# Kernel tuning notes

Hardware: AMD Instinct MI355X
Metric: run time of the kernel (lower is better)

## Reference

```python
import math
import jax, jax.numpy as jnp
import numpy as np

B, N, D, E = 4, 256, 256, 128  # batch, nodes, node_dim, edge_dim


def setup_inputs() -> dict:
    key = jax.random.key(0)
    ks = jax.random.split(key, 12)
    s_d = 1.0 / math.sqrt(D)
    s_e = 1.0 / math.sqrt(E)
    s_3d = 1.0 / math.sqrt(3 * D)
    return {
        "h": jax.random.normal(ks[0], (B, N, D), jnp.float32),
        "g": jax.random.normal(ks[1], (B, N, N, E), jnp.float32),
        "node_mask": jnp.ones((B, N), dtype=bool),
        # attention projections (stored as (in, out); x @ W == torch Linear)
        "Wq": jax.random.normal(ks[2], (D, D), jnp.float32) * s_d,
        "Wk": jax.random.normal(ks[3], (E, D), jnp.float32) * s_e,
        "Wv": jax.random.normal(ks[4], (E, D), jnp.float32) * s_e,
        # edge_to_node MLP: Linear(D,D) -> SiLU -> Linear(D,D)
        "W1a": jax.random.normal(ks[5], (D, D), jnp.float32) * s_d,
        "b1a": jnp.zeros((D,), jnp.float32),
        "W2a": jax.random.normal(ks[6], (D, D), jnp.float32) * s_d,
        "b2a": jnp.zeros((D,), jnp.float32),
        # node_to_edge MLP: Linear(3D,E) -> SiLU -> Linear(E,E)
        "W1b": jax.random.normal(ks[7], (3 * D, E), jnp.float32) * s_3d,
        "b1b": jnp.zeros((E,), jnp.float32),
        "W2b": jax.random.normal(ks[8], (E, E), jnp.float32) * s_e,
        "b2b": jnp.zeros((E,), jnp.float32),
    }


def reference(h, g, node_mask, Wq, Wk, Wv, W1a, b1a, W2a, b2a, W1b, b1b, W2b, b2b):
    scale = 1.0 / math.sqrt(D)
    # Edge-to-Node attention
    q = h @ Wq                                   # (B,N,D)
    k = jnp.einsum('bije,ed->bijd', g, Wk)       # (B,N,N,D)
    v = jnp.einsum('bije,ed->bijd', g, Wv)       # (B,N,N,D)
    scores = jnp.einsum('bid,bijd->bij', q, k) * scale
    edge_mask = node_mask[:, :, None] & node_mask[:, None, :]
    scores = jnp.where(edge_mask, scores, -10000.0)
    alpha = jax.nn.softmax(scores, axis=2)
    alpha = alpha * node_mask[:, :, None].astype(alpha.dtype)
    node_agg = jnp.einsum('bij,bijd->bid', alpha, v)
    # edge_to_node MLP (dropout = identity at inference)
    h_update = h + (jax.nn.silu(node_agg @ W1a + b1a) @ W2a + b2a)
    # Node-to-Edge: split W1b so the (B,N,N,3D) concat is never materialized;
    # pair @ W1b == h_i @ Wi + h_j @ Wj + (h_i*h_j) @ Wh  (mathematically identical)
    Wi, Wj, Wh = W1b[:D], W1b[D:2 * D], W1b[2 * D:]
    xi = (h_update @ Wi)[:, :, None, :]          # (B,N,1,E)
    xj = (h_update @ Wj)[:, None, :, :]          # (B,1,N,E)
    had = h_update[:, :, None, :] * h_update[:, None, :, :]  # (B,N,N,D)
    pre = xi + xj + jnp.einsum('bijd,de->bije', had, Wh) + b1b
    g_update = g + (jax.nn.silu(pre) @ W2b + b2b)
    return (h_update, g_update)
```

## Files before the change

### kernel.cpp

```cpp
#include <hip/hip_runtime.h>

typedef unsigned short u16;
typedef short short8 __attribute__((ext_vector_type(8)));
typedef float f32x4 __attribute__((ext_vector_type(4)));

#define DEV __device__ __forceinline__

DEV float bf2f(u16 u) { return __uint_as_float(((unsigned int)u) << 16); }
DEV u16 f2bf(float f) {
    unsigned int u = __float_as_uint(f);
    u += 0x7fffu + ((u >> 16) & 1u);
    return (u16)(u >> 16);
}
DEV unsigned cvtpk_bf16(float lo, float hi) {
    unsigned r;
    asm("v_cvt_pk_bf16_f32 %0, %1, %2" : "=v"(r) : "v"(lo), "v"(hi));
    return r;
}
DEV float sigf(float x) { return 1.0f / (1.0f + __expf(-x)); }

__global__ __launch_bounds__(256) void k_prep_t(const float* __restrict__ W1b,
                                                const float* __restrict__ W2b,
                                                u16* __restrict__ WhT,
                                                u16* __restrict__ W2bT) {
    __shared__ u16 sT[64 * 72];
    int t = threadIdx.x, blk = blockIdx.x;
    const float* src;
    u16* dst;
    int R, C, ri, ci;
    if (blk < 8) {
        src = W1b + 512 * 128;
        dst = WhT;
        R = 256; C = 128;
        ri = blk >> 1; ci = blk & 1;
    } else {
        src = W2b; dst = W2bT; R = 128; C = 128;
        int lb = blk - 8;
        ri = lb >> 1; ci = lb & 1;
    }
    int lr = t >> 2, q = t & 3;
#pragma unroll
    for (int s4 = 0; s4 < 4; ++s4) {
        float4 v = *(const float4*)(src + (size_t)(ri * 64 + lr) * C + ci * 64 + q * 16 + s4 * 4);
        int c0 = q * 16 + s4 * 4;
        sT[(c0 + 0) * 72 + lr] = f2bf(v.x);
        sT[(c0 + 1) * 72 + lr] = f2bf(v.y);
        sT[(c0 + 2) * 72 + lr] = f2bf(v.z);
        sT[(c0 + 3) * 72 + lr] = f2bf(v.w);
    }
    __syncthreads();
    int dr = t >> 2;
#pragma unroll
    for (int s8 = 0; s8 < 2; ++s8) {
        int cc = q * 16 + s8 * 8;
        ushort4 w0, w1;
        w0.x = sT[dr * 72 + cc + 0]; w0.y = sT[dr * 72 + cc + 1];
        w0.z = sT[dr * 72 + cc + 2]; w0.w = sT[dr * 72 + cc + 3];
        w1.x = sT[dr * 72 + cc + 4]; w1.y = sT[dr * 72 + cc + 5];
        w1.z = sT[dr * 72 + cc + 6]; w1.w = sT[dr * 72 + cc + 7];
        *(ushort4*)(dst + (size_t)(ci * 64 + dr) * R + ri * 64 + cc) = w0;
        *(ushort4*)(dst + (size_t)(ci * 64 + dr) * R + ri * 64 + cc + 4) = w1;
    }
}

__global__ __launch_bounds__(128) void k_prep_m1(const float* __restrict__ Wq,
                                                 const float* __restrict__ Wk,
                                                 float* __restrict__ M1) {
    __shared__ float swq[256];
    int t = threadIdx.x, c = blockIdx.x;
    swq[t] = Wq[c * 256 + t];
    swq[t + 128] = Wq[c * 256 + t + 128];
    __syncthreads();
    const float* wk = Wk + (size_t)t * 256;
    float acc = 0.f;
#pragma unroll 4
    for (int d = 0; d < 256; d += 4) {
        float4 b = *(const float4*)(wk + d);
        acc += swq[d] * b.x + swq[d + 1] * b.y + swq[d + 2] * b.z + swq[d + 3] * b.w;
    }
    M1[c * 128 + t] = acc;
}

__global__ __launch_bounds__(256) void k_prep_m2(const float* __restrict__ Wv,
                                                 const float* __restrict__ W1a,
                                                 float* __restrict__ M2) {
    __shared__ float sv[256];
    int t = threadIdx.x, e = blockIdx.x;
    sv[t] = Wv[(size_t)e * 256 + t];
    __syncthreads();
    float acc = 0.f;
#pragma unroll 16
    for (int d = 0; d < 256; ++d) acc += sv[d] * W1a[d * 256 + t];
    M2[e * 256 + t] = acc;
}

__global__ __launch_bounds__(256) void k_qk(const float* __restrict__ h,
                                            const float* __restrict__ M1,
                                            float* __restrict__ qk) {
    __shared__ float sh[2][256];
    __shared__ float sp[2][2][128];
    int t = threadIdx.x;
    int r0 = blockIdx.x * 2;
    sh[0][t] = h[(size_t)r0 * 256 + t];
    sh[1][t] = h[(size_t)(r0 + 1) * 256 + t];
    __syncthreads();
    int e = t & 127, ch = t >> 7;
    float a0 = 0.f, a1 = 0.f;
    const float* m1 = M1 + (size_t)ch * 128 * 128;
    const float* s0 = &sh[0][ch * 128];
    const float* s1 = &sh[1][ch * 128];
#pragma unroll 16
    for (int c = 0; c < 128; ++c) {
        float m = m1[c * 128 + e];
        a0 += s0[c] * m;
        a1 += s1[c] * m;
    }
    sp[ch][0][e] = a0;
    sp[ch][1][e] = a1;
    __syncthreads();
    if (t < 128) qk[(size_t)r0 * 128 + t] = sp[0][0][t] + sp[1][0][t];
    else qk[(size_t)(r0 + 1) * 128 + (t - 128)] = sp[0][1][t - 128] + sp[1][1][t - 128];
}

__global__ __launch_bounds__(256) void k_attn(const float* __restrict__ g,
                                              const float* __restrict__ qk,
                                              float* __restrict__ gagg) {
    __shared__ __align__(16) u16 sg[32768];
    __shared__ float sqk[128];
    __shared__ float ssc[256];
    __shared__ float sred[4];
    __shared__ float sacc[512];
    int t = threadIdx.x, bi = blockIdx.x;
    int lane = t & 63, wv = t >> 6;
    if (t < 128) sqk[t] = qk[bi * 128 + t] * 0.0625f;
    const float* gb = g + (size_t)bi * 32768;
#pragma unroll
    for (int it = 0; it < 32; ++it) {
        int idx = (it * 256 + t) * 4;
        float4 v = *(const float4*)(gb + idx);
        ushort4 pk;
        pk.x = f2bf(v.x); pk.y = f2bf(v.y); pk.z = f2bf(v.z); pk.w = f2bf(v.w);
        *(ushort4*)(sg + idx) = pk;
    }
    __syncthreads();

    float s = 0.f;
#pragma unroll 8
    for (int it = 0; it < 64; ++it) {
        int p2 = (it + t) & 63;
        unsigned int u = *(const unsigned int*)(sg + t * 128 + 2 * p2);
        float2 qv = *(const float2*)(sqk + 2 * p2);
        s += bf2f((u16)(u & 0xffffu)) * qv.x + bf2f((u16)(u >> 16)) * qv.y;
    }

    float v = s;
#pragma unroll
    for (int off = 32; off > 0; off >>= 1) v = fmaxf(v, __shfl_xor(v, off));
    if (lane == 0) sred[wv] = v;
    __syncthreads();
    float m = fmaxf(fmaxf(sred[0], sred[1]), fmaxf(sred[2], sred[3]));
    float pv = __expf(s - m);
    ssc[t] = pv;
    float sv = pv;
#pragma unroll
    for (int off = 32; off > 0; off >>= 1) sv += __shfl_xor(sv, off);
    __syncthreads();
    if (lane == 0) sred[wv] = sv;
    __syncthreads();
    float s_sum = sred[0] + sred[1] + sred[2] + sred[3];

    int epair = t & 63, jq = t >> 6;
    float a0 = 0.f, a1 = 0.f;
    const u16* sq = sg + jq * 8192 + 2 * epair;
#pragma unroll 8
    for (int jj = 0; jj < 64; ++jj) {
        unsigned int u = *(const unsigned int*)(sq + jj * 128);
        float p = ssc[jq * 64 + jj];
        a0 += p * bf2f((u16)(u & 0xffffu));
        a1 += p * bf2f((u16)(u >> 16));
    }
    sacc[jq * 128 + 2 * epair] = a0;
    sacc[jq * 128 + 2 * epair + 1] = a1;
    __syncthreads();
    if (t < 128)
        gagg[bi * 128 + t] = (sacc[t] + sacc[128 + t] + sacc[256 + t] + sacc[384 + t]) / s_sum;
}

__global__ __launch_bounds__(256) void k_hmlp(
    const float* __restrict__ h, const float* __restrict__ gagg,
    const float* __restrict__ M2, const float* __restrict__ b1a,
    const float* __restrict__ W2a, const float* __restrict__ b2a,
    const float* __restrict__ W1b, const float* __restrict__ b1b,
    float* __restrict__ hu_ws, u16* __restrict__ hub_ws,
    float* __restrict__ xi_ws, float* __restrict__ xj_ws,
    float* __restrict__ out) {
    __shared__ float sgg[2][128];
    __shared__ float su[2][256];
    __shared__ float shu[2][256];
    int t = threadIdx.x;
    int r0 = blockIdx.x * 2;
    sgg[t >> 7][t & 127] = gagg[(size_t)(r0 + (t >> 7)) * 128 + (t & 127)];
    __syncthreads();
    float a0 = b1a[t], a1 = a0;
#pragma unroll 16
    for (int e = 0; e < 128; ++e) {
        float mm = M2[e * 256 + t];
        a0 += sgg[0][e] * mm;
        a1 += sgg[1][e] * mm;
    }
    su[0][t] = a0 * sigf(a0);
    su[1][t] = a1 * sigf(a1);
    __syncthreads();
    float b2av = b2a[t];
    float h0 = h[(size_t)r0 * 256 + t] + b2av;
    float h1 = h[(size_t)(r0 + 1) * 256 + t] + b2av;
#pragma unroll 16
    for (int c = 0; c < 256; ++c) {
        float mm = W2a[c * 256 + t];
        h0 += su[0][c] * mm;
        h1 += su[1][c] * mm;
    }
    shu[0][t] = h0;
    shu[1][t] = h1;
    hu_ws[(size_t)r0 * 256 + t] = h0;
    hu_ws[(size_t)(r0 + 1) * 256 + t] = h1;
    hub_ws[(size_t)r0 * 256 + t] = f2bf(h0);
    hub_ws[(size_t)(r0 + 1) * 256 + t] = f2bf(h1);
    out[(size_t)r0 * 256 + t] = h0;
    out[(size_t)(r0 + 1) * 256 + t] = h1;
    __syncthreads();
    int e = t & 127, which = t >> 7;
    const float* Wp = W1b + (size_t)which * 32768;
    float x0 = which ? 0.f : b1b[e];
    float x1 = x0;
#pragma unroll 16
    for (int c = 0; c < 256; ++c) {
        float mm = Wp[c * 128 + e];
        x0 += shu[0][c] * mm;
        x1 += shu[1][c] * mm;
    }
    float* dst = which ? xj_ws : xi_ws;
    dst[(size_t)r0 * 128 + e] = x0;
    dst[(size_t)(r0 + 1) * 128 + e] = x1;
}

__global__ __launch_bounds__(256, 4) void k_gupd(
    const float* __restrict__ g, const float* __restrict__ hu_ws,
    const u16* __restrict__ hub_ws,
    const float* __restrict__ xi_ws, const float* __restrict__ xj_ws,
    const u16* __restrict__ WhT, const u16* __restrict__ W2bT,
    const float* __restrict__ b2b, float* __restrict__ out) {
    __shared__ __align__(16) u16 sP[128 * 136];
    __shared__ float s_hui[256];
    __shared__ float s_xi[128];

    int t = threadIdx.x;
    int bi = blockIdx.x;
    int jb = blockIdx.y;
    int b = bi >> 8;
    int j0 = jb * 128;
    int w = t >> 6, lane = t & 63, n = lane & 15, quad = lane >> 4;

    s_hui[t] = hu_ws[(size_t)bi * 256 + t];
    if (t < 128) s_xi[t] = xi_ws[(size_t)bi * 128 + t];
    __syncthreads();

    int jr = w * 32 + quad * 4;

    const float* xjp = xj_ws + (size_t)(b * 256 + j0) * 128;
    f32x4 acc[2][8];
#pragma unroll
    for (int mti = 0; mti < 2; ++mti)
#pragma unroll
        for (int et = 0; et < 8; ++et) {
            int e = et * 16 + n;
            float xiv = s_xi[e];
#pragma unroll
            for (int r = 0; r < 4; ++r)
                acc[mti][et][r] = xiv + xjp[(size_t)(jr + mti * 16 + r) * 128 + e];
        }

    const u16* hub = hub_ws + (size_t)(b * 256 + j0) * 256;
    int row0 = w * 32 + n;
#pragma unroll
    for (int kc = 0; kc < 4; ++kc) {
#pragma unroll
        for (int s = 0; s < 2; ++s) {
            int c0 = kc * 64 + s * 32 + quad * 8;
            short8 hj0 = *(const short8*)(hub + (size_t)row0 * 256 + c0);
            short8 hj1 = *(const short8*)(hub + (size_t)(row0 + 16) * 256 + c0);
            float4 hA = *(const float4*)(s_hui + c0);
            float4 hB = *(const float4*)(s_hui + c0 + 4);
            float hi8[8] = {hA.x, hA.y, hA.z, hA.w, hB.x, hB.y, hB.z, hB.w};
            union { short8 s8; unsigned u[4]; } a0v, a1v;
#pragma unroll
            for (int k = 0; k < 4; ++k) {
                a0v.u[k] = cvtpk_bf16(bf2f((u16)hj0[2 * k]) * hi8[2 * k],
                                      bf2f((u16)hj0[2 * k + 1]) * hi8[2 * k + 1]);
                a1v.u[k] = cvtpk_bf16(bf2f((u16)hj1[2 * k]) * hi8[2 * k],
                                      bf2f((u16)hj1[2 * k + 1]) * hi8[2 * k + 1]);
            }
#pragma unroll
            for (int et = 0; et < 8; ++et) {
                short8 bfr = *(const short8*)(WhT + (size_t)(et * 16 + n) * 256 + c0);
                acc[0][et] = __builtin_amdgcn_mfma_f32_16x16x32_bf16(a0v.s8, bfr, acc[0][et], 0, 0, 0);
                acc[1][et] = __builtin_amdgcn_mfma_f32_16x16x32_bf16(a1v.s8, bfr, acc[1][et], 0, 0, 0);
            }
        }
    }

#pragma unroll
    for (int mti = 0; mti < 2; ++mti)
#pragma unroll
        for (int et = 0; et < 8; ++et)
#pragma unroll
            for (int r = 0; r < 4; ++r) {
                float x = acc[mti][et][r];
                sP[(w * 32 + mti * 16 + quad * 4 + r) * 136 + et * 16 + n] = f2bf(x * sigf(x));
            }
    __syncthreads();

#pragma unroll
    for (int et = 0; et < 8; ++et) {
        float bv = b2b[et * 16 + n];
        f32x4 iv = {bv, bv, bv, bv};
        acc[0][et] = iv;
        acc[1][et] = iv;
    }
#pragma unroll
    for (int ks = 0; ks < 4; ++ks) {
        int f0 = ks * 32;
        short8 a0 = *(const short8*)(sP + (w * 32 + n) * 136 + f0 + quad * 8);
        short8 a1 = *(const short8*)(sP + (w * 32 + 16 + n) * 136 + f0 + quad * 8);
#pragma unroll
        for (int et = 0; et < 8; ++et) {
            short8 bfr = *(const short8*)(W2bT + (size_t)(et * 16 + n) * 128 + f0 + quad * 8);
            acc[0][et] = __builtin_amdgcn_mfma_f32_16x16x32_bf16(a0, bfr, acc[0][et], 0, 0, 0);
            acc[1][et] = __builtin_amdgcn_mfma_f32_16x16x32_bf16(a1, bfr, acc[1][et], 0, 0, 0);
        }
    }

    const float* gbase = g + ((size_t)bi * 256 + j0) * 128;
    float* obase = out + 262144 + ((size_t)bi * 256 + j0) * 128;
#pragma unroll
    for (int mti = 0; mti < 2; ++mti) {
        float gv[32];
#pragma unroll
        for (int et = 0; et < 8; ++et)
#pragma unroll
            for (int r = 0; r < 4; ++r)
                gv[et * 4 + r] = gbase[(size_t)(jr + mti * 16 + r) * 128 + et * 16 + n];
#pragma unroll
        for (int et = 0; et < 8; ++et)
#pragma unroll
            for (int r = 0; r < 4; ++r)
                obase[(size_t)(jr + mti * 16 + r) * 128 + et * 16 + n] =
                    gv[et * 4 + r] + acc[mti][et][r];
    }
}

extern "C" void kernel_launch(void* const* d_in, const int* in_sizes, int n_in,
                              void* d_out, int out_size, void* d_ws, size_t ws_size,
                              hipStream_t stream) {
    const float* h   = (const float*)d_in[0];
    const float* g   = (const float*)d_in[1];
    const float* Wq  = (const float*)d_in[3];
    const float* Wk  = (const float*)d_in[4];
    const float* Wv  = (const float*)d_in[5];
    const float* W1a = (const float*)d_in[6];
    const float* b1a = (const float*)d_in[7];
    const float* W2a = (const float*)d_in[8];
    const float* b2a = (const float*)d_in[9];
    const float* W1b = (const float*)d_in[10];
    const float* b1b = (const float*)d_in[11];
    const float* W2b = (const float*)d_in[12];
    const float* b2b = (const float*)d_in[13];

    float* ws   = (float*)d_ws;
    float* M1   = ws;
    float* M2   = M1 + 32768;
    float* qk   = M2 + 32768;
    float* xj   = qk;
    float* gagg = qk + 131072;
    float* hu   = gagg + 131072;
    float* xi   = hu + 262144;
    u16* hub    = (u16*)(xi + 131072);
    u16* WhT    = hub + 262144;
    u16* W2bT   = WhT + 32768;

    float* out = (float*)d_out;

    k_prep_t<<<12, 256, 0, stream>>>(W1b, W2b, WhT, W2bT);
    k_prep_m1<<<256, 128, 0, stream>>>(Wq, Wk, M1);
    k_prep_m2<<<128, 256, 0, stream>>>(Wv, W1a, M2);
    k_qk<<<512, 256, 0, stream>>>(h, M1, qk);
    k_attn<<<1024, 256, 0, stream>>>(g, qk, gagg);
    k_hmlp<<<512, 256, 0, stream>>>(h, gagg, M2, b1a, W2a, b2a, W1b, b1b,
                                    hu, hub, xi, xj, out);
    k_gupd<<<dim3(1024, 2), 256, 0, stream>>>(g, hu, hub, xi, xj, WhT, W2bT, b2b, out);
}
```

Baseline: 454.0 us.

## Fold xj projection into gupd MFMA loop and stage g-update epilogue through LDS

The h_j @ Wj term is no longer precomputed in fp32 by the node MLP kernel and reloaded per tile. It is now computed inside the edge-update kernel with extra bf16 MFMAs against a newly transposed WjT, reusing the already-loaded h_j fragments. This removes the scattered fp32 xj loads, at the cost of extra MFMA work per tile and bf16 precision for that term. Separately, the final g + delta write now stages the accumulators through shared memory, so global g reads and output writes become coalesced float4 accesses. That costs extra barriers and shared-memory traffic.

```diff
diff --git a/kernel.cpp b/kernel.cpp
--- a/kernel.cpp
+++ b/kernel.cpp
@@ -22,20 +22,23 @@
 __global__ __launch_bounds__(256) void k_prep_t(const float* __restrict__ W1b,
                                                 const float* __restrict__ W2b,
                                                 u16* __restrict__ WhT,
+                                                u16* __restrict__ WjT,
                                                 u16* __restrict__ W2bT) {
     __shared__ u16 sT[64 * 72];
     int t = threadIdx.x, blk = blockIdx.x;
     const float* src;
     u16* dst;
     int R, C, ri, ci;
-    if (blk < 8) {
-        src = W1b + 512 * 128;
-        dst = WhT;
+    if (blk < 16) {
+        int m = blk >> 3;
+        src = W1b + (m ? 256 * 128 : 512 * 128);
+        dst = m ? WjT : WhT;
         R = 256; C = 128;
-        ri = blk >> 1; ci = blk & 1;
+        int lb = blk & 7;
+        ri = lb >> 1; ci = lb & 1;
     } else {
         src = W2b; dst = W2bT; R = 128; C = 128;
-        int lb = blk - 8;
+        int lb = blk - 16;
         ri = lb >> 1; ci = lb & 1;
     }
     int lr = t >> 2, q = t & 3;
@@ -192,8 +195,7 @@
     const float* __restrict__ W2a, const float* __restrict__ b2a,
     const float* __restrict__ W1b, const float* __restrict__ b1b,
     float* __restrict__ hu_ws, u16* __restrict__ hub_ws,
-    float* __restrict__ xi_ws, float* __restrict__ xj_ws,
-    float* __restrict__ out) {
+    float* __restrict__ xi_ws, float* __restrict__ out) {
     __shared__ float sgg[2][128];
     __shared__ float su[2][256];
     __shared__ float shu[2][256];
@@ -229,28 +231,22 @@
     out[(size_t)r0 * 256 + t] = h0;
     out[(size_t)(r0 + 1) * 256 + t] = h1;
     __syncthreads();
-    int e = t & 127, which = t >> 7;
-    const float* Wp = W1b + (size_t)which * 32768;
-    float x0 = which ? 0.f : b1b[e];
-    float x1 = x0;
+    int e = t & 127, row = t >> 7;
+    float x = b1b[e];
 #pragma unroll 16
-    for (int c = 0; c < 256; ++c) {
-        float mm = Wp[c * 128 + e];
-        x0 += shu[0][c] * mm;
-        x1 += shu[1][c] * mm;
-    }
-    float* dst = which ? xj_ws : xi_ws;
-    dst[(size_t)r0 * 128 + e] = x0;
-    dst[(size_t)(r0 + 1) * 128 + e] = x1;
+    for (int c = 0; c < 256; ++c) x += shu[row][c] * W1b[c * 128 + e];
+    xi_ws[(size_t)(r0 + row) * 128 + e] = x;
 }
 
 __global__ __launch_bounds__(256, 4) void k_gupd(
     const float* __restrict__ g, const float* __restrict__ hu_ws,
-    const u16* __restrict__ hub_ws,
-    const float* __restrict__ xi_ws, const float* __restrict__ xj_ws,
-    const u16* __restrict__ WhT, const u16* __restrict__ W2bT,
-    const float* __restrict__ b2b, float* __restrict__ out) {
-    __shared__ __align__(16) u16 sP[128 * 136];
+    const u16* __restrict__ hub_ws, const float* __restrict__ xi_ws,
+    const u16* __restrict__ WhT, const u16* __restrict__ WjT,
+    const u16* __restrict__ W2bT, const float* __restrict__ b2b,
+    float* __restrict__ out) {
+    __shared__ __align__(16) char uni[34816];
+    u16* sP = (u16*)uni;
+    float* sF = (float*)uni;
     __shared__ float s_hui[256];
     __shared__ float s_xi[128];
 
@@ -267,18 +263,14 @@
 
     int jr = w * 32 + quad * 4;
 
-    const float* xjp = xj_ws + (size_t)(b * 256 + j0) * 128;
     f32x4 acc[2][8];
 #pragma unroll
-    for (int mti = 0; mti < 2; ++mti)
-#pragma unroll
-        for (int et = 0; et < 8; ++et) {
-            int e = et * 16 + n;
-            float xiv = s_xi[e];
-#pragma unroll
-            for (int r = 0; r < 4; ++r)
-                acc[mti][et][r] = xiv + xjp[(size_t)(jr + mti * 16 + r) * 128 + e];
-        }
+    for (int et = 0; et < 8; ++et) {
+        float xiv = s_xi[et * 16 + n];
+        f32x4 iv = {xiv, xiv, xiv, xiv};
+        acc[0][et] = iv;
+        acc[1][et] = iv;
+    }
 
     const u16* hub = hub_ws + (size_t)(b * 256 + j0) * 256;
     int row0 = w * 32 + n;
@@ -289,6 +281,12 @@
             int c0 = kc * 64 + s * 32 + quad * 8;
             short8 hj0 = *(const short8*)(hub + (size_t)row0 * 256 + c0);
             short8 hj1 = *(const short8*)(hub + (size_t)(row0 + 16) * 256 + c0);
+#pragma unroll
+            for (int et = 0; et < 8; ++et) {
+                short8 bfr = *(const short8*)(WjT + (size_t)(et * 16 + n) * 256 + c0);
+                acc[0][et] = __builtin_amdgcn_mfma_f32_16x16x32_bf16(hj0, bfr, acc[0][et], 0, 0, 0);
+                acc[1][et] = __builtin_amdgcn_mfma_f32_16x16x32_bf16(hj1, bfr, acc[1][et], 0, 0, 0);
+            }
             float4 hA = *(const float4*)(s_hui + c0);
             float4 hB = *(const float4*)(s_hui + c0 + 4);
             float hi8[8] = {hA.x, hA.y, hA.z, hA.w, hB.x, hB.y, hB.z, hB.w};
@@ -318,7 +316,6 @@
                 float x = acc[mti][et][r];
                 sP[(w * 32 + mti * 16 + quad * 4 + r) * 136 + et * 16 + n] = f2bf(x * sigf(x));
             }
-    __syncthreads();
 
 #pragma unroll
     for (int et = 0; et < 8; ++et) {
@@ -344,18 +341,26 @@
     float* obase = out + 262144 + ((size_t)bi * 256 + j0) * 128;
 #pragma unroll
     for (int mti = 0; mti < 2; ++mti) {
-        float gv[32];
+        __syncthreads();
 #pragma unroll
         for (int et = 0; et < 8; ++et)
 #pragma unroll
             for (int r = 0; r < 4; ++r)
-                gv[et * 4 + r] = gbase[(size_t)(jr + mti * 16 + r) * 128 + et * 16 + n];
-#pragma unroll
-        for (int et = 0; et < 8; ++et)
-#pragma unroll
-            for (int r = 0; r < 4; ++r)
-                obase[(size_t)(jr + mti * 16 + r) * 128 + et * 16 + n] =
-                    gv[et * 4 + r] + acc[mti][et][r];
+                sF[(w * 16 + quad * 4 + r) * 132 + et * 16 + n] = acc[mti][et][r];
+        __syncthreads();
+#pragma unroll
+        for (int it = 0; it < 8; ++it) {
+            int fidx = it * 256 + t;
+            int rp = fidx >> 5;
+            int c4 = fidx & 31;
+            int jrow = (rp >> 4) * 32 + mti * 16 + (rp & 15);
+            float4 gv = *(const float4*)(gbase + (size_t)jrow * 128 + c4 * 4);
+            float4 pv2 = *(const float4*)(sF + rp * 132 + c4 * 4);
+            float4 ov;
+            ov.x = gv.x + pv2.x; ov.y = gv.y + pv2.y;
+            ov.z = gv.z + pv2.z; ov.w = gv.w + pv2.w;
+            *(float4*)(obase + (size_t)jrow * 128 + c4 * 4) = ov;
+        }
     }
 }
 
@@ -380,22 +385,22 @@
     float* M1   = ws;
     float* M2   = M1 + 32768;
     float* qk   = M2 + 32768;
-    float* xj   = qk;
     float* gagg = qk + 131072;
     float* hu   = gagg + 131072;
     float* xi   = hu + 262144;
     u16* hub    = (u16*)(xi + 131072);
     u16* WhT    = hub + 262144;
-    u16* W2bT   = WhT + 32768;
+    u16* WjT    = WhT + 32768;
+    u16* W2bT   = WjT + 32768;
 
     float* out = (float*)d_out;
 
-    k_prep_t<<<12, 256, 0, stream>>>(W1b, W2b, WhT, W2bT);
+    k_prep_t<<<20, 256, 0, stream>>>(W1b, W2b, WhT, WjT, W2bT);
     k_prep_m1<<<256, 128, 0, stream>>>(Wq, Wk, M1);
     k_prep_m2<<<128, 256, 0, stream>>>(Wv, W1a, M2);
     k_qk<<<512, 256, 0, stream>>>(h, M1, qk);
     k_attn<<<1024, 256, 0, stream>>>(g, qk, gagg);
     k_hmlp<<<512, 256, 0, stream>>>(h, gagg, M2, b1a, W2a, b2a, W1b, b1b,
-                                    hu, hub, xi, xj, out);
-    k_gupd<<<dim3(1024, 2), 256, 0, stream>>>(g, hu, hub, xi, xj, WhT, W2bT, b2b, out);
-}
+                                    hu, hub, xi, out);
+    k_gupd<<<dim3(1024, 2), 256, 0, stream>>>(g, hu, hub, xi, WhT, WjT, W2bT, b2b, out);
+}
```

Result: slower. 506.5 us (+11.6%).

## Stage Wh and xj tiles in LDS and coalesce g residual writes in gupd

Applied to the files above, without the earlier changes.

The Wh weight is re-laid out in per-64-column tiles so k_gupd can stage each K-chunk in shared memory, prefetching the next chunk into registers while the MFMAs run. xj is stored as bf16 and staged through LDS, and the final g + update epilogue goes through a shared float tile so global reads and writes become coalesced float4 accesses. k_attn uses packed bf16 conversion instructions. Occupancy hint drops from 4 to 3 blocks because of the larger LDS footprint, and extra barriers are added.

```diff
diff --git a/kernel.cpp b/kernel.cpp
--- a/kernel.cpp
+++ b/kernel.cpp
@@ -27,14 +27,15 @@
     int t = threadIdx.x, blk = blockIdx.x;
     const float* src;
     u16* dst;
-    int R, C, ri, ci;
+    int C, ri, ci;
+    bool tiled;
     if (blk < 8) {
         src = W1b + 512 * 128;
         dst = WhT;
-        R = 256; C = 128;
+        C = 128; tiled = true;
         ri = blk >> 1; ci = blk & 1;
     } else {
-        src = W2b; dst = W2bT; R = 128; C = 128;
+        src = W2b; dst = W2bT; C = 128; tiled = false;
         int lb = blk - 8;
         ri = lb >> 1; ci = lb & 1;
     }
@@ -58,8 +59,14 @@
         w0.z = sT[dr * 72 + cc + 2]; w0.w = sT[dr * 72 + cc + 3];
         w1.x = sT[dr * 72 + cc + 4]; w1.y = sT[dr * 72 + cc + 5];
         w1.z = sT[dr * 72 + cc + 6]; w1.w = sT[dr * 72 + cc + 7];
-        *(ushort4*)(dst + (size_t)(ci * 64 + dr) * R + ri * 64 + cc) = w0;
-        *(ushort4*)(dst + (size_t)(ci * 64 + dr) * R + ri * 64 + cc + 4) = w1;
+        size_t di;
+        if (tiled) {
+            di = (size_t)ri * 8192 + (size_t)(ci * 64 + dr) * 64 + cc;
+        } else {
+            di = (size_t)(ci * 64 + dr) * 128 + ri * 64 + cc;
+        }
+        *(ushort4*)(dst + di) = w0;
+        *(ushort4*)(dst + di + 4) = w1;
     }
 }
 
@@ -138,9 +145,10 @@
     for (int it = 0; it < 32; ++it) {
         int idx = (it * 256 + t) * 4;
         float4 v = *(const float4*)(gb + idx);
-        ushort4 pk;
-        pk.x = f2bf(v.x); pk.y = f2bf(v.y); pk.z = f2bf(v.z); pk.w = f2bf(v.w);
-        *(ushort4*)(sg + idx) = pk;
+        uint2 pk;
+        pk.x = cvtpk_bf16(v.x, v.y);
+        pk.y = cvtpk_bf16(v.z, v.w);
+        *(uint2*)(sg + idx) = pk;
     }
     __syncthreads();
 
@@ -192,7 +200,7 @@
     const float* __restrict__ W2a, const float* __restrict__ b2a,
     const float* __restrict__ W1b, const float* __restrict__ b1b,
     float* __restrict__ hu_ws, u16* __restrict__ hub_ws,
-    float* __restrict__ xi_ws, float* __restrict__ xj_ws,
+    float* __restrict__ xi_ws, u16* __restrict__ xjb_ws,
     float* __restrict__ out) {
     __shared__ float sgg[2][128];
     __shared__ float su[2][256];
@@ -239,18 +247,26 @@
         x0 += shu[0][c] * mm;
         x1 += shu[1][c] * mm;
     }
-    float* dst = which ? xj_ws : xi_ws;
-    dst[(size_t)r0 * 128 + e] = x0;
-    dst[(size_t)(r0 + 1) * 128 + e] = x1;
-}
-
-__global__ __launch_bounds__(256, 4) void k_gupd(
+    if (which) {
+        xjb_ws[(size_t)r0 * 128 + e] = f2bf(x0);
+        xjb_ws[(size_t)(r0 + 1) * 128 + e] = f2bf(x1);
+    } else {
+        xi_ws[(size_t)r0 * 128 + e] = x0;
+        xi_ws[(size_t)(r0 + 1) * 128 + e] = x1;
+    }
+}
+
+__global__ __launch_bounds__(256, 3) void k_gupd(
     const float* __restrict__ g, const float* __restrict__ hu_ws,
-    const u16* __restrict__ hub_ws,
-    const float* __restrict__ xi_ws, const float* __restrict__ xj_ws,
+    const u16* __restrict__ hub_ws, const float* __restrict__ xi_ws,
+    const u16* __restrict__ xjb_ws,
     const u16* __restrict__ WhT, const u16* __restrict__ W2bT,
     const float* __restrict__ b2b, float* __restrict__ out) {
-    __shared__ __align__(16) u16 sP[128 * 136];
+    __shared__ __align__(16) char uni[52224];
+    u16* sW  = (u16*)uni;
+    u16* sXJ = (u16*)(uni + 18432);
+    u16* sP  = (u16*)(uni + 18432);
+    float* sF = (float*)(uni + 18432);
     __shared__ float s_hui[256];
     __shared__ float s_xi[128];
 
@@ -263,11 +279,25 @@
 
     s_hui[t] = hu_ws[(size_t)bi * 256 + t];
     if (t < 128) s_xi[t] = xi_ws[(size_t)bi * 128 + t];
+
+    const u16* xjp = xjb_ws + (size_t)(b * 256 + j0) * 128;
+    short8 stg[4];
+    int se = t >> 3, sc8 = t & 7;
+#pragma unroll
+    for (int it = 0; it < 4; ++it)
+        stg[it] = *(const short8*)(WhT + (size_t)(it * 256 + t) * 8);
+#pragma unroll
+    for (int it = 0; it < 8; ++it) {
+        int f = it * 256 + t;
+        short8 v = *(const short8*)(xjp + (size_t)f * 8);
+        *(short8*)(sXJ + (f >> 4) * 132 + (f & 15) * 8) = v;
+    }
+#pragma unroll
+    for (int it = 0; it < 4; ++it)
+        *(short8*)(sW + (se + it * 32) * 72 + sc8 * 8) = stg[it];
     __syncthreads();
 
     int jr = w * 32 + quad * 4;
-
-    const float* xjp = xj_ws + (size_t)(b * 256 + j0) * 128;
     f32x4 acc[2][8];
 #pragma unroll
     for (int mti = 0; mti < 2; ++mti)
@@ -277,16 +307,22 @@
             float xiv = s_xi[e];
 #pragma unroll
             for (int r = 0; r < 4; ++r)
-                acc[mti][et][r] = xiv + xjp[(size_t)(jr + mti * 16 + r) * 128 + e];
+                acc[mti][et][r] = xiv + bf2f(sXJ[(jr + mti * 16 + r) * 132 + e]);
         }
 
     const u16* hub = hub_ws + (size_t)(b * 256 + j0) * 256;
     int row0 = w * 32 + n;
-#pragma unroll
     for (int kc = 0; kc < 4; ++kc) {
+        if (kc < 3) {
+            const u16* whp = WhT + (kc + 1) * 8192;
+#pragma unroll
+            for (int it = 0; it < 4; ++it)
+                stg[it] = *(const short8*)(whp + (size_t)(it * 256 + t) * 8);
+        }
 #pragma unroll
         for (int s = 0; s < 2; ++s) {
             int c0 = kc * 64 + s * 32 + quad * 8;
+            int cb = s * 32 + quad * 8;
             short8 hj0 = *(const short8*)(hub + (size_t)row0 * 256 + c0);
             short8 hj1 = *(const short8*)(hub + (size_t)(row0 + 16) * 256 + c0);
             float4 hA = *(const float4*)(s_hui + c0);
@@ -302,11 +338,18 @@
             }
 #pragma unroll
             for (int et = 0; et < 8; ++et) {
-                short8 bfr = *(const short8*)(WhT + (size_t)(et * 16 + n) * 256 + c0);
+                short8 bfr = *(const short8*)(sW + (et * 16 + n) * 72 + cb);
                 acc[0][et] = __builtin_amdgcn_mfma_f32_16x16x32_bf16(a0v.s8, bfr, acc[0][et], 0, 0, 0);
                 acc[1][et] = __builtin_amdgcn_mfma_f32_16x16x32_bf16(a1v.s8, bfr, acc[1][et], 0, 0, 0);
             }
         }
+        __syncthreads();
+        if (kc < 3) {
+#pragma unroll
+            for (int it = 0; it < 4; ++it)
+                *(short8*)(sW + (se + it * 32) * 72 + sc8 * 8) = stg[it];
+            __syncthreads();
+        }
     }
 
 #pragma unroll
@@ -316,9 +359,8 @@
 #pragma unroll
             for (int r = 0; r < 4; ++r) {
                 float x = acc[mti][et][r];
-                sP[(w * 32 + mti * 16 + quad * 4 + r) * 136 + et * 16 + n] = f2bf(x * sigf(x));
+                sP[(w * 32 + mti * 16 + quad * 4 + r) * 132 + et * 16 + n] = f2bf(x * sigf(x));
             }
-    __syncthreads();
 
 #pragma unroll
     for (int et = 0; et < 8; ++et) {
@@ -330,8 +372,8 @@
 #pragma unroll
     for (int ks = 0; ks < 4; ++ks) {
         int f0 = ks * 32;
-        short8 a0 = *(const short8*)(sP + (w * 32 + n) * 136 + f0 + quad * 8);
-        short8 a1 = *(const short8*)(sP + (w * 32 + 16 + n) * 136 + f0 + quad * 8);
+        short8 a0 = *(const short8*)(sP + (w * 32 + n) * 132 + f0 + quad * 8);
+        short8 a1 = *(const short8*)(sP + (w * 32 + 16 + n) * 132 + f0 + quad * 8);
 #pragma unroll
         for (int et = 0; et < 8; ++et) {
             short8 bfr = *(const short8*)(W2bT + (size_t)(et * 16 + n) * 128 + f0 + quad * 8);
@@ -344,18 +386,26 @@
     float* obase = out + 262144 + ((size_t)bi * 256 + j0) * 128;
 #pragma unroll
     for (int mti = 0; mti < 2; ++mti) {
-        float gv[32];
+        __syncthreads();
 #pragma unroll
         for (int et = 0; et < 8; ++et)
 #pragma unroll
             for (int r = 0; r < 4; ++r)
-                gv[et * 4 + r] = gbase[(size_t)(jr + mti * 16 + r) * 128 + et * 16 + n];
-#pragma unroll
-        for (int et = 0; et < 8; ++et)
-#pragma unroll
-            for (int r = 0; r < 4; ++r)
-                obase[(size_t)(jr + mti * 16 + r) * 128 + et * 16 + n] =
-                    gv[et * 4 + r] + acc[mti][et][r];
+                sF[(w * 16 + quad * 4 + r) * 132 + et * 16 + n] = acc[mti][et][r];
+        __syncthreads();
+#pragma unroll
+        for (int it = 0; it < 8; ++it) {
+            int fidx = it * 256 + t;
+            int rp = fidx >> 5;
+            int c4 = fidx & 31;
+            int jrow = (rp >> 4) * 32 + mti * 16 + (rp & 15);
+            float4 gv = *(const float4*)(gbase + (size_t)jrow * 128 + c4 * 4);
+            float4 pv2 = *(const float4*)(sF + rp * 132 + c4 * 4);
+            float4 ov;
+            ov.x = gv.x + pv2.x; ov.y = gv.y + pv2.y;
+            ov.z = gv.z + pv2.z; ov.w = gv.w + pv2.w;
+            *(float4*)(obase + (size_t)jrow * 128 + c4 * 4) = ov;
+        }
     }
 }
 
@@ -380,13 +430,13 @@
     float* M1   = ws;
     float* M2   = M1 + 32768;
     float* qk   = M2 + 32768;
-    float* xj   = qk;
     float* gagg = qk + 131072;
     float* hu   = gagg + 131072;
     float* xi   = hu + 262144;
     u16* hub    = (u16*)(xi + 131072);
     u16* WhT    = hub + 262144;
     u16* W2bT   = WhT + 32768;
+    u16* xjb    = W2bT + 16384;
 
     float* out = (float*)d_out;
 
@@ -396,6 +446,6 @@
     k_qk<<<512, 256, 0, stream>>>(h, M1, qk);
     k_attn<<<1024, 256, 0, stream>>>(g, qk, gagg);
     k_hmlp<<<512, 256, 0, stream>>>(h, gagg, M2, b1a, W2a, b2a, W1b, b1b,
-                                    hu, hub, xi, xj, out);
-    k_gupd<<<dim3(1024, 2), 256, 0, stream>>>(g, hu, hub, xi, xj, WhT, W2bT, b2b, out);
-}
+                                    hu, hub, xi, xjb, out);
+    k_gupd<<<dim3(1024, 2), 256, 0, stream>>>(g, hu, hub, xi, xjb, WhT, W2bT, b2b, out);
+}
```

Measured after the change: 374.1 us. -17.6%, faster.
